# Optimization experiments

Measured on AMD Instinct MI355X. Metric: run time of the kernel, lower is better.

Reference implementation:

```python
import jax, jax.numpy as jnp
import numpy as np

HIDDEN = 2048
NUM_HEADS = 8
NUM_KV_HEADS = 1
HEAD_DIM = 256
ROPE_THETA = 10000.0
T = 2048  # num tokens (single causal prefill sequence)
Q_SIZE = NUM_HEADS * HEAD_DIM        # 2048
KV_SIZE = NUM_KV_HEADS * HEAD_DIM    # 256


def _apply_rope(x, positions):
    # x: [T, n_heads, head_dim], neox style (rotate halves)
    half = HEAD_DIM // 2
    inv_freq = 1.0 / (ROPE_THETA ** (jnp.arange(half, dtype=jnp.float32) * 2.0 / HEAD_DIM))
    ang = positions.astype(jnp.float32)[:, None] * inv_freq[None, :]   # [T, half]
    cos = jnp.cos(ang)[:, None, :]
    sin = jnp.sin(ang)[:, None, :]
    x1, x2 = jnp.split(x, 2, axis=-1)
    return jnp.concatenate([x1 * cos - x2 * sin, x2 * cos + x1 * sin], axis=-1)


def setup_inputs() -> dict:
    key = jax.random.key(0)
    k1, k2, k3 = jax.random.split(key, 3)
    hidden_states = jax.random.normal(k1, (T, HIDDEN), dtype=jnp.float32)
    Wqkv = jax.random.normal(k2, (Q_SIZE + 2 * KV_SIZE, HIDDEN), dtype=jnp.float32) * 0.02
    Wo = jax.random.normal(k3, (HIDDEN, Q_SIZE), dtype=jnp.float32) * 0.02
    positions = jnp.arange(T, dtype=jnp.int32)
    return {"positions": positions, "hidden_states": hidden_states, "Wqkv": Wqkv, "Wo": Wo}


def reference(positions, hidden_states, Wqkv, Wo):
    scaling = HEAD_DIM ** -0.5
    qkv = hidden_states @ Wqkv.T                                   # [T, Q+2KV]
    q = qkv[:, :Q_SIZE].reshape(T, NUM_HEADS, HEAD_DIM)
    k = qkv[:, Q_SIZE:Q_SIZE + KV_SIZE].reshape(T, NUM_KV_HEADS, HEAD_DIM)
    v = qkv[:, Q_SIZE + KV_SIZE:].reshape(T, NUM_KV_HEADS, HEAD_DIM)
    q = _apply_rope(q, positions)
    k = _apply_rope(k, positions)
    # GQA: group query heads over kv heads
    g = NUM_HEADS // NUM_KV_HEADS
    qg = q.reshape(T, NUM_KV_HEADS, g, HEAD_DIM)
    scores = jnp.einsum('qhgd,khd->hgqk', qg, k) * scaling         # [kv, g, T, T]
    causal = jnp.arange(T)[:, None] >= jnp.arange(T)[None, :]
    scores = jnp.where(causal[None, None], scores, jnp.finfo(scores.dtype).min)
    probs = jax.nn.softmax(scores, axis=-1)
    attn = jnp.einsum('hgqk,khd->qhgd', probs, v).reshape(T, Q_SIZE)
    return attn @ Wo.T
```

## Files before the change

### kernel.cpp

```cpp
#include <hip/hip_runtime.h>
#include <hip/hip_bf16.h>

typedef __bf16 bf16x8 __attribute__((ext_vector_type(8)));
typedef __bf16 bf16x4 __attribute__((ext_vector_type(4)));
typedef float floatx4 __attribute__((ext_vector_type(4)));

__device__ __forceinline__ float fast_exp2(float x) {
    return __builtin_amdgcn_exp2f(x);
}

__device__ __forceinline__ void lds_barrier() {
    asm volatile("s_waitcnt lgkmcnt(0)\n\ts_barrier" ::: "memory");
}

__global__ __launch_bounds__(256) void cast_all(const float* __restrict__ hid,
                                                const float* __restrict__ wqkv,
                                                const float* __restrict__ wo,
                                                __bf16* __restrict__ Ah,
                                                __bf16* __restrict__ Wqkvh,
                                                __bf16* __restrict__ Woh) {
    const int n1 = 1048576, n2 = 1310720;
    int i = blockIdx.x * 256 + threadIdx.x;
    const float* in;
    __bf16* out;
    int j;
    if (i < n1) { in = hid; out = Ah; j = i; }
    else if (i < n1 + n2) { in = wqkv; out = Wqkvh; j = i - n1; }
    else { in = wo; out = Woh; j = i - n1 - n2; }
    float4 v = ((const float4*)in)[j];
    bf16x4 o;
    o[0] = (__bf16)v.x; o[1] = (__bf16)v.y; o[2] = (__bf16)v.z; o[3] = (__bf16)v.w;
    ((bf16x4*)out)[j] = o;
}

template<typename OutT>
__global__ __launch_bounds__(256) void gemm_bt(const __bf16* __restrict__ A,
                                               const __bf16* __restrict__ B,
                                               OutT* __restrict__ C,
                                               int M, int N, int K) {
    __shared__ __attribute__((aligned(16))) __bf16 As[128 * 64];
    __shared__ __attribute__((aligned(16))) __bf16 Bs[128 * 64];

    int tid = threadIdx.x, lane = tid & 63, w = tid >> 6;
    int wm = (w >> 1) * 64, wn = (w & 1) * 64;
    int bm0 = blockIdx.x * 128, bn0 = blockIdx.y * 128;
    int r = lane & 15, q4 = lane >> 4;
    int rr = lane >> 2, qq = lane & 3;

    const __bf16* Agp[4];
    const __bf16* Bgp[4];
    __bf16* Asd[4];
    __bf16* Bsd[4];
#pragma unroll
    for (int j = 0; j < 4; j++) {
        int c = w * 4 + j;
        int kk = c >> 3, g = c & 7;
        Agp[j] = A + (size_t)(bm0 + g * 16 + rr) * K + kk * 32 + qq * 8;
        Bgp[j] = B + (size_t)(bn0 + g * 16 + rr) * K + kk * 32 + qq * 8;
        Asd[j] = &As[c * 512 + lane * 8];
        Bsd[j] = &Bs[c * 512 + lane * 8];
    }

    floatx4 acc[4][4];
#pragma unroll
    for (int i = 0; i < 4; i++)
#pragma unroll
        for (int j = 0; j < 4; j++) acc[i][j] = (floatx4)0.f;

    bf16x8 ar[4], br[4];
#pragma unroll
    for (int j = 0; j < 4; j++) {
        ar[j] = *(const bf16x8*)Agp[j];
        br[j] = *(const bf16x8*)Bgp[j];
    }

    for (int k0 = 0; k0 < K; k0 += 64) {
        lds_barrier();
#pragma unroll
        for (int j = 0; j < 4; j++) {
            *(bf16x8*)Asd[j] = ar[j];
            *(bf16x8*)Bsd[j] = br[j];
        }
        if (k0 + 64 < K) {
#pragma unroll
            for (int j = 0; j < 4; j++) {
                ar[j] = *(const bf16x8*)(Agp[j] + k0 + 64);
                br[j] = *(const bf16x8*)(Bgp[j] + k0 + 64);
            }
        }
        lds_barrier();

#pragma unroll
        for (int kk = 0; kk < 2; kk++) {
            bf16x8 a[4], b[4];
#pragma unroll
            for (int mt = 0; mt < 4; mt++)
                a[mt] = *(const bf16x8*)&As[(kk * 8 + (wm >> 4) + mt) * 512 + r * 32 + q4 * 8];
#pragma unroll
            for (int nt = 0; nt < 4; nt++)
                b[nt] = *(const bf16x8*)&Bs[(kk * 8 + (wn >> 4) + nt) * 512 + r * 32 + q4 * 8];
#pragma unroll
            for (int mt = 0; mt < 4; mt++)
#pragma unroll
                for (int nt = 0; nt < 4; nt++)
                    acc[mt][nt] = __builtin_amdgcn_mfma_f32_16x16x32_bf16(a[mt], b[nt], acc[mt][nt], 0, 0, 0);
        }
    }

#pragma unroll
    for (int mt = 0; mt < 4; mt++)
#pragma unroll
        for (int nt = 0; nt < 4; nt++) {
            int row = bm0 + wm + mt * 16 + q4 * 4;
            int col = bn0 + wn + nt * 16 + r;
#pragma unroll
            for (int i = 0; i < 4; i++)
                C[(size_t)(row + i) * N + col] = (OutT)acc[mt][nt][i];
        }
}

__global__ __launch_bounds__(256) void rope_vtrans(const __bf16* __restrict__ qkv,
                                                   const int* __restrict__ positions,
                                                   __bf16* __restrict__ Qo,
                                                   __bf16* __restrict__ Ko,
                                                   __bf16* __restrict__ Vt) {
    __shared__ float tile[32][33];
    int b = blockIdx.x;
    if (b < 9216) {
        int idx = b * 256 + threadIdx.x;
        int i = idx & 127;
        int th = idx >> 7;
        int head = th % 9;
        int t = th / 9;
        float invf = expf(-(float)i * 0.07195578415606394f);
        float ang = (float)positions[t] * invf;
        float s = sinf(ang), c = cosf(ang);
        size_t off = (size_t)t * 2560 + (head < 8 ? head * 256 : 2048);
        float x1 = (float)qkv[off + i];
        float x2 = (float)qkv[off + i + 128];
        if (head < 8) {
            const float qs = 0.09016844f;
            __bf16* dst = Qo + (size_t)t * 2048 + head * 256;
            dst[i]       = (__bf16)((x1 * c - x2 * s) * qs);
            dst[i + 128] = (__bf16)((x2 * c + x1 * s) * qs);
        } else {
            __bf16* dst = Ko + (size_t)t * 256;
            dst[i]       = (__bf16)(x1 * c - x2 * s);
            dst[i + 128] = (__bf16)(x2 * c + x1 * s);
        }
    } else {
        int bb = b - 9216;
        int bt = bb & 63;
        int bc = bb >> 6;
        int tx = threadIdx.x & 31;
        int ty0 = threadIdx.x >> 5;
#pragma unroll
        for (int ty = ty0; ty < 32; ty += 8)
            tile[ty][tx] = (float)qkv[(size_t)(bt * 32 + ty) * 2560 + 2304 + bc * 32 + tx];
        __syncthreads();
#pragma unroll
        for (int ty = ty0; ty < 32; ty += 8)
            Vt[(size_t)bt * 8192 + (bc * 32 + ty) * 32 + tx] = (__bf16)tile[tx][ty];
    }
}

__global__ __launch_bounds__(256) void attn_kernel(const __bf16* __restrict__ Q,
                                                   const __bf16* __restrict__ Kg,
                                                   const __bf16* __restrict__ Vt,
                                                   __bf16* __restrict__ Opart,
                                                   float2* __restrict__ Ml) {
    __shared__ __attribute__((aligned(16))) __bf16 Ks[32 * 264];
    __shared__ __attribute__((aligned(16))) __bf16 Vs[16 * 512];
    __shared__ __attribute__((aligned(16))) __bf16 Ps[4][16][40];

    int hg = blockIdx.x;
    int rs = 407 - (int)blockIdx.y;
    int k, base;
    if (rs < 24)       { k = 1; base = 0; }
    else if (rs < 72)  { k = 2; base = 24; }
    else if (rs < 144) { k = 3; base = 72; }
    else if (rs < 240) { k = 4; base = 144; }
    else if (rs < 360) { k = 5; base = 240; }
    else               { k = 6; base = 360; }
    int idx = rs - base;
    int s = idx % k;
    int g = (k - 1) * 24 + idx / k;
    int slot = base + idx - s;

    int start = s * 384;
    int end = g * 16 + 16;
    if (end > start + 384) end = start + 384;
    int ntiles = (end - start + 31) >> 5;

    int tid = threadIdx.x, lane = tid & 63, w = tid >> 6;
    int r = lane & 15, q4 = lane >> 4;
    int h = hg * 4 + w;

    int krow = w * 8 + (lane & 7);
    int kcol = (lane >> 3) * 32;
    __bf16* kd = &Ks[krow * 264 + kcol];
    __bf16* vd = &Vs[(tid >> 4) * 512 + (tid & 15) * 8];
    const __bf16* vgp = Vt + (size_t)tid * 32;

    bf16x8 qf[8];
    {
        const __bf16* qrow = Q + (size_t)(g * 16 + r) * 2048 + h * 256 + q4 * 8;
#pragma unroll
        for (int ks = 0; ks < 8; ks++) qf[ks] = *(const bf16x8*)(qrow + ks * 32);
    }

    bf16x8 ones;
#pragma unroll
    for (int i = 0; i < 8; i++) ones[i] = (__bf16)1.0f;

    floatx4 acc[16];
#pragma unroll
    for (int i = 0; i < 16; i++) acc[i] = (floatx4)0.f;
    floatx4 acc_l = (floatx4)0.f;

    bf16x8 kr[4], vr[4];
    {
        const __bf16* kp = Kg + (size_t)(start + krow) * 256 + kcol;
        const __bf16* vp = vgp + (size_t)(start >> 5) * 8192;
#pragma unroll
        for (int j = 0; j < 4; j++) {
            kr[j] = *(const bf16x8*)(kp + j * 8);
            vr[j] = *(const bf16x8*)(vp + j * 8);
        }
    }

    for (int t = 0; t < ntiles; t++) {
        int kt0 = start + t * 32;
        lds_barrier();
#pragma unroll
        for (int j = 0; j < 4; j++) {
            *(bf16x8*)(kd + j * 8) = kr[j];
            *(bf16x8*)(vd + j * 128) = vr[j];
        }
        if (t + 1 < ntiles) {
            const __bf16* kp = Kg + (size_t)(kt0 + 32 + krow) * 256 + kcol;
            const __bf16* vp = vgp + (size_t)((kt0 + 32) >> 5) * 8192;
#pragma unroll
            for (int j = 0; j < 4; j++) {
                kr[j] = *(const bf16x8*)(kp + j * 8);
                vr[j] = *(const bf16x8*)(vp + j * 8);
            }
        }
        lds_barrier();

        floatx4 sc[2];
        sc[0] = (floatx4)0.f; sc[1] = (floatx4)0.f;
#pragma unroll
        for (int ks = 0; ks < 8; ks++) {
#pragma unroll
            for (int nt = 0; nt < 2; nt++) {
                bf16x8 kf = *(const bf16x8*)&Ks[(nt * 16 + r) * 264 + ks * 32 + q4 * 8];
                sc[nt] = __builtin_amdgcn_mfma_f32_16x16x32_bf16(qf[ks], kf, sc[nt], 0, 0, 0);
            }
        }
        if (kt0 + 31 > g * 16) {
            int qbase = g * 16 + q4 * 4;
#pragma unroll
            for (int nt = 0; nt < 2; nt++) {
                int kpos = kt0 + nt * 16 + r;
#pragma unroll
                for (int i = 0; i < 4; i++)
                    if (kpos > qbase + i) sc[nt][i] = -3e38f;
            }
        }

#pragma unroll
        for (int nt = 0; nt < 2; nt++)
#pragma unroll
            for (int i = 0; i < 4; i++)
                Ps[w][q4 * 4 + i][(nt * 16 + r) ^ (q4 << 3)] = (__bf16)fast_exp2(sc[nt][i]);
        __builtin_amdgcn_wave_barrier();
        bf16x8 pf = *(const bf16x8*)&Ps[w][r][(q4 * 8) ^ ((r >> 2) << 3)];
        __builtin_amdgcn_wave_barrier();

#pragma unroll
        for (int n16 = 0; n16 < 16; n16++) {
            bf16x8 vf = *(const bf16x8*)&Vs[n16 * 512 + lane * 8];
            acc[n16] = __builtin_amdgcn_mfma_f32_16x16x32_bf16(pf, vf, acc[n16], 0, 0, 0);
        }
        acc_l = __builtin_amdgcn_mfma_f32_16x16x32_bf16(pf, ones, acc_l, 0, 0, 0);
    }

    size_t base_row = (size_t)(slot + s) * 128 + hg * 64 + w * 16;
#pragma unroll
    for (int n16 = 0; n16 < 16; n16++)
#pragma unroll
        for (int i = 0; i < 4; i++)
            Opart[(base_row + q4 * 4 + i) * 256 + n16 * 16 + r] = (__bf16)acc[n16][i];
    if (r == 0) {
#pragma unroll
        for (int i = 0; i < 4; i++)
            Ml[base_row + q4 * 4 + i] = make_float2(0.f, acc_l[i]);
    }
}

__global__ __launch_bounds__(256) void combine_kernel(const __bf16* __restrict__ Opart,
                                                      const float2* __restrict__ Ml,
                                                      __bf16* __restrict__ attnb) {
    int wid = blockIdx.x * 4 + (threadIdx.x >> 6);
    int lane = threadIdx.x & 63;
    int t = wid >> 3, h = wid & 7;
    int g = t >> 4, row = t & 15;
    int hg = h >> 2, w = h & 3;
    int nsp = g / 24 + 1;
    int full = g / 24, rem = g % 24;
    int fg = 12 * full * (full + 1) + rem * (full + 1);

    float ms[6], ls[6];
    size_t rbase[6];
    float M = -3e38f;
    for (int s = 0; s < nsp; s++) {
        rbase[s] = (size_t)(fg + s) * 128 + hg * 64 + w * 16 + row;
        float2 ml = Ml[rbase[s]];
        ms[s] = ml.x; ls[s] = ml.y;
        M = fmaxf(M, ml.x);
    }
    float L = 0.f;
    float o[4] = {0.f, 0.f, 0.f, 0.f};
    for (int s = 0; s < nsp; s++) {
        float wsc = fast_exp2(ms[s] - M);
        L += ls[s] * wsc;
        bf16x4 v = *(const bf16x4*)&Opart[rbase[s] * 256 + lane * 4];
#pragma unroll
        for (int j = 0; j < 4; j++) o[j] += wsc * (float)v[j];
    }
    float inv = 1.f / L;
    bf16x4 ov;
#pragma unroll
    for (int j = 0; j < 4; j++) ov[j] = (__bf16)(o[j] * inv);
    *(bf16x4*)&attnb[(size_t)t * 2048 + h * 256 + lane * 4] = ov;
}

extern "C" void kernel_launch(void* const* d_in, const int* in_sizes, int n_in,
                              void* d_out, int out_size, void* d_ws, size_t ws_size,
                              hipStream_t stream) {
    const int* positions = (const int*)d_in[0];
    const float* hidden  = (const float*)d_in[1];
    const float* Wqkv    = (const float*)d_in[2];
    const float* Wo      = (const float*)d_in[3];
    float* out = (float*)d_out;

    char* ws = (char*)d_ws;
    const size_t MB = 1024 * 1024;
    __bf16* Ah    = (__bf16*)(ws + 0 * MB);
    __bf16* Woh   = (__bf16*)(ws + 8 * MB);
    __bf16* Qb    = (__bf16*)(ws + 16 * MB);
    __bf16* Kb    = (__bf16*)(ws + 24 * MB);
    __bf16* Vtb   = (__bf16*)(ws + 25 * MB);
    __bf16* Wqkvh = (__bf16*)(ws + 26 * MB);
    __bf16* qkvb  = (__bf16*)(ws + 36 * MB);
    __bf16* Opart = (__bf16*)(ws + 26 * MB);
    float2* Ml    = (float2*)(ws + 52 * MB);
    __bf16* attnb = Ah;

    cast_all<<<13312, 256, 0, stream>>>(hidden, Wqkv, Wo, Ah, Wqkvh, Woh);

    gemm_bt<__bf16><<<dim3(16, 20), 256, 0, stream>>>(Ah, Wqkvh, qkvb, 2048, 2560, 2048);

    rope_vtrans<<<9728, 256, 0, stream>>>(qkvb, positions, Qb, Kb, Vtb);

    attn_kernel<<<dim3(2, 408), 256, 0, stream>>>(Qb, Kb, Vtb, Opart, Ml);
    combine_kernel<<<4096, 256, 0, stream>>>(Opart, Ml, attnb);

    gemm_bt<float><<<dim3(16, 16), 256, 0, stream>>>(attnb, Woh, out, 2048, 2048, 2048);
}
```

Measured before the change: 236.2 us.

## Split-K both GEMMs in two halves and fold partial sums downstream

Both projection GEMMs now split the K dimension in two via blockIdx.z, doubling the block count so more of the GPU's compute units have work. The QKV partials are summed inside the rope/V-transpose kernel, and a new add_out kernel sums the output-projection partials into float. The combine kernel also drops the per-split max rescaling, since the attention kernel always writes a zero max. In exchange it writes and re-reads bf16 partial buffers, adds one extra launch, and rounds each partial sum to bf16, which loses some precision.

```diff
diff --git a/kernel.cpp b/kernel.cpp
--- a/kernel.cpp
+++ b/kernel.cpp
@@ -33,11 +33,10 @@
     ((bf16x4*)out)[j] = o;
 }
 
-template<typename OutT>
-__global__ __launch_bounds__(256) void gemm_bt(const __bf16* __restrict__ A,
-                                               const __bf16* __restrict__ B,
-                                               OutT* __restrict__ C,
-                                               int M, int N, int K) {
+__global__ __launch_bounds__(256) void gemm_bt_splitk(const __bf16* __restrict__ A,
+                                                      const __bf16* __restrict__ B,
+                                                      __bf16* __restrict__ C,
+                                                      int M, int N, int K) {
     __shared__ __attribute__((aligned(16))) __bf16 As[128 * 64];
     __shared__ __attribute__((aligned(16))) __bf16 Bs[128 * 64];
 
@@ -46,6 +45,8 @@
     int bm0 = blockIdx.x * 128, bn0 = blockIdx.y * 128;
     int r = lane & 15, q4 = lane >> 4;
     int rr = lane >> 2, qq = lane & 3;
+    int Khalf = K >> 1;
+    int kbase = (int)blockIdx.z * Khalf;
 
     const __bf16* Agp[4];
     const __bf16* Bgp[4];
@@ -55,8 +56,8 @@
     for (int j = 0; j < 4; j++) {
         int c = w * 4 + j;
         int kk = c >> 3, g = c & 7;
-        Agp[j] = A + (size_t)(bm0 + g * 16 + rr) * K + kk * 32 + qq * 8;
-        Bgp[j] = B + (size_t)(bn0 + g * 16 + rr) * K + kk * 32 + qq * 8;
+        Agp[j] = A + (size_t)(bm0 + g * 16 + rr) * K + kbase + kk * 32 + qq * 8;
+        Bgp[j] = B + (size_t)(bn0 + g * 16 + rr) * K + kbase + kk * 32 + qq * 8;
         Asd[j] = &As[c * 512 + lane * 8];
         Bsd[j] = &Bs[c * 512 + lane * 8];
     }
@@ -74,14 +75,14 @@
         br[j] = *(const bf16x8*)Bgp[j];
     }
 
-    for (int k0 = 0; k0 < K; k0 += 64) {
+    for (int k0 = 0; k0 < Khalf; k0 += 64) {
         lds_barrier();
 #pragma unroll
         for (int j = 0; j < 4; j++) {
             *(bf16x8*)Asd[j] = ar[j];
             *(bf16x8*)Bsd[j] = br[j];
         }
-        if (k0 + 64 < K) {
+        if (k0 + 64 < Khalf) {
 #pragma unroll
             for (int j = 0; j < 4; j++) {
                 ar[j] = *(const bf16x8*)(Agp[j] + k0 + 64);
@@ -107,6 +108,7 @@
         }
     }
 
+    __bf16* Cp = C + (size_t)blockIdx.z * M * N;
 #pragma unroll
     for (int mt = 0; mt < 4; mt++)
 #pragma unroll
@@ -115,11 +117,12 @@
             int col = bn0 + wn + nt * 16 + r;
 #pragma unroll
             for (int i = 0; i < 4; i++)
-                C[(size_t)(row + i) * N + col] = (OutT)acc[mt][nt][i];
-        }
-}
-
-__global__ __launch_bounds__(256) void rope_vtrans(const __bf16* __restrict__ qkv,
+                Cp[(size_t)(row + i) * N + col] = (__bf16)acc[mt][nt][i];
+        }
+}
+
+__global__ __launch_bounds__(256) void rope_vtrans(const __bf16* __restrict__ qa,
+                                                   const __bf16* __restrict__ qb,
                                                    const int* __restrict__ positions,
                                                    __bf16* __restrict__ Qo,
                                                    __bf16* __restrict__ Ko,
@@ -136,8 +139,8 @@
         float ang = (float)positions[t] * invf;
         float s = sinf(ang), c = cosf(ang);
         size_t off = (size_t)t * 2560 + (head < 8 ? head * 256 : 2048);
-        float x1 = (float)qkv[off + i];
-        float x2 = (float)qkv[off + i + 128];
+        float x1 = (float)qa[off + i] + (float)qb[off + i];
+        float x2 = (float)qa[off + i + 128] + (float)qb[off + i + 128];
         if (head < 8) {
             const float qs = 0.09016844f;
             __bf16* dst = Qo + (size_t)t * 2048 + head * 256;
@@ -155,8 +158,10 @@
         int tx = threadIdx.x & 31;
         int ty0 = threadIdx.x >> 5;
 #pragma unroll
-        for (int ty = ty0; ty < 32; ty += 8)
-            tile[ty][tx] = (float)qkv[(size_t)(bt * 32 + ty) * 2560 + 2304 + bc * 32 + tx];
+        for (int ty = ty0; ty < 32; ty += 8) {
+            size_t gi = (size_t)(bt * 32 + ty) * 2560 + 2304 + bc * 32 + tx;
+            tile[ty][tx] = (float)qa[gi] + (float)qb[gi];
+        }
         __syncthreads();
 #pragma unroll
         for (int ty = ty0; ty < 32; ty += 8)
@@ -311,29 +316,41 @@
     int full = g / 24, rem = g % 24;
     int fg = 12 * full * (full + 1) + rem * (full + 1);
 
-    float ms[6], ls[6];
+    float ls[6];
     size_t rbase[6];
-    float M = -3e38f;
     for (int s = 0; s < nsp; s++) {
         rbase[s] = (size_t)(fg + s) * 128 + hg * 64 + w * 16 + row;
-        float2 ml = Ml[rbase[s]];
-        ms[s] = ml.x; ls[s] = ml.y;
-        M = fmaxf(M, ml.x);
+        ls[s] = Ml[rbase[s]].y;
     }
     float L = 0.f;
     float o[4] = {0.f, 0.f, 0.f, 0.f};
     for (int s = 0; s < nsp; s++) {
-        float wsc = fast_exp2(ms[s] - M);
-        L += ls[s] * wsc;
+        L += ls[s];
         bf16x4 v = *(const bf16x4*)&Opart[rbase[s] * 256 + lane * 4];
 #pragma unroll
-        for (int j = 0; j < 4; j++) o[j] += wsc * (float)v[j];
+        for (int j = 0; j < 4; j++) o[j] += (float)v[j];
     }
     float inv = 1.f / L;
     bf16x4 ov;
 #pragma unroll
     for (int j = 0; j < 4; j++) ov[j] = (__bf16)(o[j] * inv);
     *(bf16x4*)&attnb[(size_t)t * 2048 + h * 256 + lane * 4] = ov;
+}
+
+__global__ __launch_bounds__(256) void add_out(const __bf16* __restrict__ p0,
+                                               const __bf16* __restrict__ p1,
+                                               float* __restrict__ out, int n4) {
+    int i = blockIdx.x * 256 + threadIdx.x;
+    if (i < n4) {
+        bf16x4 a = ((const bf16x4*)p0)[i];
+        bf16x4 b = ((const bf16x4*)p1)[i];
+        float4 o;
+        o.x = (float)a[0] + (float)b[0];
+        o.y = (float)a[1] + (float)b[1];
+        o.z = (float)a[2] + (float)b[2];
+        o.w = (float)a[3] + (float)b[3];
+        ((float4*)out)[i] = o;
+    }
 }
 
 extern "C" void kernel_launch(void* const* d_in, const int* in_sizes, int n_in,
@@ -353,19 +370,23 @@
     __bf16* Kb    = (__bf16*)(ws + 24 * MB);
     __bf16* Vtb   = (__bf16*)(ws + 25 * MB);
     __bf16* Wqkvh = (__bf16*)(ws + 26 * MB);
-    __bf16* qkvb  = (__bf16*)(ws + 36 * MB);
+    __bf16* qkvp  = (__bf16*)(ws + 36 * MB);
+    __bf16* qkv_a = qkvp;
+    __bf16* qkv_b = qkvp + (size_t)2048 * 2560;
     __bf16* Opart = (__bf16*)(ws + 26 * MB);
     float2* Ml    = (float2*)(ws + 52 * MB);
     __bf16* attnb = Ah;
+    __bf16* gp    = (__bf16*)(ws + 26 * MB);
 
     cast_all<<<13312, 256, 0, stream>>>(hidden, Wqkv, Wo, Ah, Wqkvh, Woh);
 
-    gemm_bt<__bf16><<<dim3(16, 20), 256, 0, stream>>>(Ah, Wqkvh, qkvb, 2048, 2560, 2048);
-
-    rope_vtrans<<<9728, 256, 0, stream>>>(qkvb, positions, Qb, Kb, Vtb);
+    gemm_bt_splitk<<<dim3(16, 20, 2), 256, 0, stream>>>(Ah, Wqkvh, qkvp, 2048, 2560, 2048);
+
+    rope_vtrans<<<9728, 256, 0, stream>>>(qkv_a, qkv_b, positions, Qb, Kb, Vtb);
 
     attn_kernel<<<dim3(2, 408), 256, 0, stream>>>(Qb, Kb, Vtb, Opart, Ml);
     combine_kernel<<<4096, 256, 0, stream>>>(Opart, Ml, attnb);
 
-    gemm_bt<float><<<dim3(16, 16), 256, 0, stream>>>(attnb, Woh, out, 2048, 2048, 2048);
-}
+    gemm_bt_splitk<<<dim3(16, 16, 2), 256, 0, stream>>>(attnb, Woh, gp, 2048, 2048, 2048);
+    add_out<<<4096, 256, 0, stream>>>(gp, gp + (size_t)2048 * 2048, out, 1048576);
+}
```

After: 226.0 us. -4.3%, faster.
